# Optimization experiments

Hardware: AMD Instinct MI355X
Metric: run time of the kernel (lower is better)

## Reference

```python
import jax, jax.numpy as jnp
import numpy as np

H = 8          # query heads
HKV = 4        # kv heads
D = 256        # head dim
GROUPS = H // HKV
HIDDEN = 2304
WINDOW = 2048  # sliding window
SOFTCAP = 50.0
SCALE = (HIDDEN // H) ** -0.5  # query_pre_attn_scalar uses hidden//heads, not head_dim
NEG = -1e9
ROPE_BASE = 10000.0


def _rope_tables(L, offset=0, dtype=jnp.float32):
    inv_freq = 1.0 / (ROPE_BASE ** (jnp.arange(0, D, 2, dtype=jnp.float32) / D))
    t = jnp.arange(offset, offset + L, dtype=jnp.float32)
    freqs = jnp.outer(t, inv_freq)                    # [L, D/2]
    emb = jnp.concatenate([freqs, freqs], axis=-1)    # [L, D]
    return jnp.cos(emb).astype(dtype), jnp.sin(emb).astype(dtype)


def _rotate_half(x):
    x1, x2 = jnp.split(x, 2, axis=-1)
    return jnp.concatenate([-x2, x1], axis=-1)


def _apply_rope(x, cos, sin):
    # x: [B, h, L, D]; cos/sin: [L, D]
    return x * cos[None, None] + _rotate_half(x) * sin[None, None]


def setup_inputs() -> dict:
    key = jax.random.key(0)
    ks = jax.random.split(key, 5)
    B, L = 1, 4096
    x = jax.random.normal(ks[0], (B, L, HIDDEN), dtype=jnp.float32)
    wq = jax.random.normal(ks[1], (HIDDEN, H * D), dtype=jnp.float32) * 0.02
    wk = jax.random.normal(ks[2], (HIDDEN, HKV * D), dtype=jnp.float32) * 0.02
    wv = jax.random.normal(ks[3], (HIDDEN, HKV * D), dtype=jnp.float32) * 0.02
    wo = jax.random.normal(ks[4], (H * D, HIDDEN), dtype=jnp.float32) * 0.02
    # additive causal mask [1,1,L,L]
    causal = jnp.triu(jnp.full((L, L), NEG, dtype=jnp.float32), k=1)
    mask = causal[None, None]
    return {"x": x, "mask": mask, "wq": wq, "wk": wk, "wv": wv, "wo": wo}


def reference(x, mask, wq, wk, wv, wo):
    B, L, _ = x.shape
    q = (x @ wq).reshape(B, L, H, D).transpose(0, 2, 1, 3)     # [B,H,L,D]
    k = (x @ wk).reshape(B, L, HKV, D).transpose(0, 2, 1, 3)   # [B,HKV,L,D]
    v = (x @ wv).reshape(B, L, HKV, D).transpose(0, 2, 1, 3)

    cos, sin = _rope_tables(L, 0, q.dtype)
    q = _apply_rope(q, cos, sin)
    k = _apply_rope(k, cos, sin)

    # GQA: repeat_interleave kv heads
    k = jnp.repeat(k, GROUPS, axis=1)  # [B,H,L,D]
    v = jnp.repeat(v, GROUPS, axis=1)

    attn = jnp.einsum("bhqd,bhkd->bhqk", q, k) * SCALE
    attn = SOFTCAP * jnp.tanh(attn / SOFTCAP)
    attn = attn + mask

    kv_len = attn.shape[-1]
    if kv_len > WINDOW:  # sliding branch: keep only last WINDOW key columns
        col_keep = jnp.arange(kv_len) >= (kv_len - WINDOW)  # [kv_len]
        attn = jnp.where(col_keep[None, None, None, :], attn, NEG)

    attn = jax.nn.softmax(attn.astype(jnp.float32), axis=-1).astype(q.dtype)
    out = jnp.einsum("bhqk,bhkd->bhqd", attn, v)
    out = out.transpose(0, 2, 1, 3).reshape(B, L, H * D)
    return out @ wo
```

## Files before the change

kernel.cpp:

```cpp
#include <hip/hip_runtime.h>

typedef unsigned short u16;
typedef __bf16 bf16x8 __attribute__((ext_vector_type(8)));
typedef float floatx4 __attribute__((ext_vector_type(4)));
typedef unsigned short u16x4 __attribute__((ext_vector_type(4)));
typedef unsigned short u16x8 __attribute__((ext_vector_type(8)));

#define L_SEQ 4096
#define HID   2304
#define NH    8
#define NKV   4
#define HD    256
#define QDIM  2048
#define KVDIM 1024
#define SCALE_F 0.05892556509887896f

__device__ __forceinline__ u16 f2bf(float f) {
  unsigned u = __float_as_uint(f);
  u += 0x7FFFu + ((u >> 16) & 1u);
  return (u16)(u >> 16);
}
__device__ __forceinline__ float bf2f(u16 h) {
  return __uint_as_float(((unsigned)h) << 16);
}

__device__ __forceinline__ void async_load16(const u16* g, u16* lds_base) {
  __builtin_amdgcn_global_load_lds(
      (const __attribute__((address_space(1))) unsigned int*)g,
      (__attribute__((address_space(3))) unsigned int*)lds_base, 16, 0, 0);
}

__device__ __forceinline__ int swz(int m) { return (m + (m >> 2)) & 3; }

__global__ __launch_bounds__(256)
void cast_kernel(const float* __restrict__ in, u16* __restrict__ out, int n4) {
  int i = blockIdx.x * 256 + threadIdx.x;
  if (i < n4) {
    float4 v = *reinterpret_cast<const float4*>(&in[(size_t)i * 4]);
    u16x4 o;
    o[0] = f2bf(v.x); o[1] = f2bf(v.y); o[2] = f2bf(v.z); o[3] = f2bf(v.w);
    *reinterpret_cast<u16x4*>(&out[(size_t)i * 4]) = o;
  }
}

__global__ __launch_bounds__(256)
void transpose_kernel(const float* __restrict__ wq, const float* __restrict__ wk,
                      const float* __restrict__ wv, const float* __restrict__ wo,
                      u16* __restrict__ wqkvT, u16* __restrict__ woT) {
  const int z = blockIdx.z;
  const float* W; u16* WT; int K, N;
  if (z == 0)      { W = wq; WT = wqkvT;                            K = HID;  N = QDIM; }
  else if (z == 1) { W = wk; WT = wqkvT + (size_t)QDIM * HID;       K = HID;  N = KVDIM; }
  else if (z == 2) { W = wv; WT = wqkvT + (size_t)(QDIM + KVDIM) * HID; K = HID; N = KVDIM; }
  else             { W = wo; WT = woT;                              K = QDIM; N = HID; }
  const int n0 = blockIdx.x * 32, k0 = blockIdx.y * 32;
  if (n0 >= N || k0 >= K) return;
  __shared__ u16 t[32][33];
  const int c = threadIdx.x & 31, r4 = (threadIdx.x >> 5) * 4;
#pragma unroll
  for (int i = 0; i < 4; ++i)
    t[r4 + i][c] = f2bf(W[(size_t)(k0 + r4 + i) * N + n0 + c]);
  __syncthreads();
#pragma unroll
  for (int i = 0; i < 4; ++i)
    WT[(size_t)(n0 + r4 + i) * K + k0 + c] = t[c][r4 + i];
}

#define G256_NT 36

#define G256_BARRIER() __builtin_amdgcn_s_barrier()
#define G256_SCHEDB()  __builtin_amdgcn_sched_barrier(0)

#define G256_STAGE(bb, X, kh, tt)                                              \
  {                                                                            \
    const u16* g = (X) ? BT + (size_t)(n0 + w * 32 + srow) * HID               \
                       : A + (size_t)(m0 + w * 32 + srow) * HID;               \
    const int kc = (tt) * 64 + (kh) * 32 + schk;                               \
    async_load16(g + kc, &lds[bb][X][kh][(w * 32) * 32]);                      \
    async_load16(g + 16 * HID + kc, &lds[bb][X][kh][(w * 32 + 16) * 32]);      \
  }

#define G256_RD_B(dst, bb, kk)                                                 \
  {                                                                            \
    const u16* Bk = &lds[bb][1][kk][0];                                        \
    _Pragma("unroll") for (int nt = 0; nt < 4; ++nt)                           \
        dst[nt] = *reinterpret_cast<const bf16x8*>(                            \
            &Bk[(wn + nt * 16 + l16) * 32 + rsw]);                             \
  }

#define G256_RD_A(dst, bb, kk, ch)                                             \
  {                                                                            \
    const u16* Ak = &lds[bb][0][kk][0];                                        \
    _Pragma("unroll") for (int mt = 0; mt < 4; ++mt)                           \
        dst[mt] = *reinterpret_cast<const bf16x8*>(                            \
            &Ak[(wm + ((ch) * 4 + mt) * 16 + l16) * 32 + rsw]);                \
  }

#define G256_MFMA(ch, AA, BB)                                                  \
  {                                                                            \
    __builtin_amdgcn_s_setprio(1);                                             \
    _Pragma("unroll") for (int mt = 0; mt < 4; ++mt)                           \
        _Pragma("unroll") for (int nt = 0; nt < 4; ++nt)                       \
            acc[(ch) * 4 + mt][nt] = __builtin_amdgcn_mfma_f32_16x16x32_bf16(  \
                AA[mt], BB[nt], acc[(ch) * 4 + mt][nt], 0, 0, 0);              \
    __builtin_amdgcn_s_setprio(0);                                             \
  }

#define G256_VMCNT4() __asm__ volatile("s_waitcnt vmcnt(4)")
#define G256_VMCNT0() __asm__ volatile("s_waitcnt vmcnt(0)")

__global__ __launch_bounds__(512)
void gemm256_kernel(const u16* __restrict__ A, const u16* __restrict__ BT,
                    u16* __restrict__ C) {
  __shared__ __align__(16) u16 lds[2][2][2][256 * 32];

  const int tid  = threadIdx.x;
  const int lane = tid & 63;
  const int w    = tid >> 6;
  const int l16  = lane & 15;
  const int quad = lane >> 4;
  const int wm   = (w >> 2) * 128;
  const int wn   = (w & 3) * 64;

  const int srow = lane >> 2;
  const int schk = (((lane & 3) ^ ((lane >> 3) & 3))) * 8;
  const int rsw = ((quad ^ ((l16 >> 1) & 3))) * 8;

  const int bid = blockIdx.x;
  const int id  = (bid & 7) * 20 + (bid >> 3);

  int m0, n0, region;
  if (id < 64)      { region = 0; n0 = (id & 7) * 256;          m0 = 2048 + (id >> 3) * 256; }
  else if (id < 96) { region = 1; const int i = id - 64;
                      n0 = 2048 + (i & 3) * 256;                m0 = 2048 + (i >> 2) * 256; }
  else              { region = 2; const int i = id - 96;
                      n0 = 3072 + (i & 3) * 256;                m0 = (i >> 2) * 256; }

  floatx4 acc[8][4];
#pragma unroll
  for (int i = 0; i < 8; ++i)
#pragma unroll
    for (int j = 0; j < 4; ++j) acc[i][j] = (floatx4){0.f, 0.f, 0.f, 0.f};

  G256_STAGE(0, 0, 0, 0); G256_STAGE(0, 1, 0, 0);
  G256_STAGE(0, 0, 1, 0); G256_STAGE(0, 1, 1, 0);
  G256_STAGE(1, 0, 0, 1); G256_STAGE(1, 1, 0, 1);
  G256_VMCNT4();
  G256_BARRIER();

#pragma unroll 2
  for (int t = 0; t < G256_NT; ++t) {
    const int bb = t & 1;
    bf16x8 a_cur[4], b_cur[4], a_hi0[4], a_lo1[4], b1[4], a_hi1[4];

    G256_RD_A(a_cur, bb, 0, 0);
    G256_RD_B(b_cur, bb, 0);
    G256_RD_A(a_hi0, bb, 0, 1);
    if (t + 1 < G256_NT) { G256_STAGE(bb ^ 1, 0, 1, t + 1); }
    G256_SCHEDB();
    G256_MFMA(0, a_cur, b_cur);
    G256_BARRIER();

    G256_RD_A(a_lo1, bb, 1, 0);
    G256_RD_B(b1, bb, 1);
    if (t + 1 < G256_NT) { G256_STAGE(bb ^ 1, 1, 1, t + 1); }
    G256_SCHEDB();
    G256_MFMA(1, a_hi0, b_cur);
    G256_BARRIER();

    G256_RD_A(a_hi1, bb, 1, 1);
    if (t + 2 < G256_NT) { G256_STAGE(bb, 0, 0, t + 2); }
    G256_SCHEDB();
    G256_MFMA(0, a_lo1, b1);
    G256_BARRIER();

    if (t + 2 < G256_NT) { G256_STAGE(bb, 1, 0, t + 2); }
    G256_SCHEDB();
    G256_MFMA(1, a_hi1, b1);
    if (t < G256_NT - 2) { G256_VMCNT4(); }
    else                 { G256_VMCNT0(); }
    G256_BARRIER();
  }

#pragma unroll
  for (int mt = 0; mt < 8; ++mt)
#pragma unroll
    for (int nt = 0; nt < 4; ++nt) {
      const int mbase = m0 + wm + mt * 16 + quad * 4;
      const int n = n0 + wn + nt * 16 + l16;
      if (region == 0) {
        const size_t base = (size_t)(n >> 8) * L_SEQ * HD + (n & 255);
#pragma unroll
        for (int r = 0; r < 4; ++r)
          C[base + (size_t)(mbase + r) * HD] = f2bf(acc[mt][nt][r]);
      } else if (region == 1) {
        const int nk2 = n - QDIM;
        const size_t base = (size_t)NH * L_SEQ * HD +
                            (size_t)(nk2 >> 8) * L_SEQ * HD + (nk2 & 255);
#pragma unroll
        for (int r = 0; r < 4; ++r)
          C[base + (size_t)(mbase + r) * HD] = f2bf(acc[mt][nt][r]);
      } else {
        const int nv = n - QDIM - KVDIM;
        u16x4 o;
#pragma unroll
        for (int r = 0; r < 4; ++r) o[r] = f2bf(acc[mt][nt][r]);
        *reinterpret_cast<u16x4*>(
            &C[(size_t)(NH + NKV) * L_SEQ * HD +
               ((size_t)(nv >> 8) * HD + (nv & 255)) * L_SEQ + mbase]) = o;
      }
    }
}

template<int MODE>
__global__ __launch_bounds__(256)
void gemm_kernel(const u16* __restrict__ A, const u16* __restrict__ BT,
                 void* __restrict__ Cp, int N, int K) {
  __shared__ __align__(16) u16 Alds[128][32];
  __shared__ __align__(16) u16 Blds[128][32];

  const int tid  = threadIdx.x;
  const int lane = tid & 63;
  const int w    = tid >> 6;
  const int wm   = (w >> 1) * 64;
  const int wn   = (w & 1) * 64;
  const int l16  = lane & 15;
  const int quad = lane >> 4;

  int m0, n0;
  if (MODE == 0) {
    const int id = blockIdx.x;
    if (id < 256)      { n0 = (id & 15) * 128;                 m0 = 2048 + (id >> 4) * 128; }
    else if (id < 384) { const int i2 = id - 256;
                         n0 = 2048 + (i2 & 7) * 128;           m0 = 2048 + (i2 >> 3) * 128; }
    else               { const int i3 = id - 384;
                         n0 = 3072 + (i3 & 7) * 128;           m0 = (i3 >> 3) * 128; }
  } else {
    m0 = blockIdx.y * 128;
    n0 = blockIdx.x * 128;
  }

  const int srow_in = lane >> 2;
  const int schunk  = lane & 3;

  floatx4 acc[4][4];
#pragma unroll
  for (int i = 0; i < 4; ++i)
#pragma unroll
    for (int j = 0; j < 4; ++j) acc[i][j] = (floatx4){0.f, 0.f, 0.f, 0.f};

  const int nk = K >> 5;
  for (int kt = 0; kt < nk; ++kt) {
    __syncthreads();
#pragma unroll
    for (int p = 0; p < 2; ++p) {
      const int row = w * 32 + p * 16 + srow_in;
      const int ce  = schunk ^ swz(row);
      async_load16(&A[(size_t)(m0 + row) * K + kt * 32 + ce * 8], &Alds[w * 32 + p * 16][0]);
      async_load16(&BT[(size_t)(n0 + row) * K + kt * 32 + ce * 8], &Blds[w * 32 + p * 16][0]);
    }
    __syncthreads();

    bf16x8 a[4], b[4];
#pragma unroll
    for (int mt = 0; mt < 4; ++mt) {
      const int row = wm + mt * 16 + l16;
      a[mt] = *reinterpret_cast<const bf16x8*>(&Alds[row][(quad ^ swz(row)) * 8]);
    }
#pragma unroll
    for (int nt = 0; nt < 4; ++nt) {
      const int row = wn + nt * 16 + l16;
      b[nt] = *reinterpret_cast<const bf16x8*>(&Blds[row][(quad ^ swz(row)) * 8]);
    }
#pragma unroll
    for (int mt = 0; mt < 4; ++mt)
#pragma unroll
      for (int nt = 0; nt < 4; ++nt)
        acc[mt][nt] = __builtin_amdgcn_mfma_f32_16x16x32_bf16(a[mt], b[nt], acc[mt][nt], 0, 0, 0);
  }

#pragma unroll
  for (int mt = 0; mt < 4; ++mt)
#pragma unroll
    for (int nt = 0; nt < 4; ++nt) {
      const int mbase = m0 + wm + mt * 16 + quad * 4;
      const int n = n0 + wn + nt * 16 + l16;
      if (MODE == 0) {
        u16* C = (u16*)Cp;
        if (n < QDIM) {
          const size_t base = (size_t)(n >> 8) * L_SEQ * HD + (n & 255);
#pragma unroll
          for (int r = 0; r < 4; ++r)
            C[base + (size_t)(mbase + r) * HD] = f2bf(acc[mt][nt][r]);
        } else if (n < QDIM + KVDIM) {
          const int nk2 = n - QDIM;
          const size_t base = (size_t)NH * L_SEQ * HD +
                              (size_t)(nk2 >> 8) * L_SEQ * HD + (nk2 & 255);
#pragma unroll
          for (int r = 0; r < 4; ++r)
            C[base + (size_t)(mbase + r) * HD] = f2bf(acc[mt][nt][r]);
        } else {
          const int nv = n - QDIM - KVDIM;
          u16x4 o;
#pragma unroll
          for (int r = 0; r < 4; ++r) o[r] = f2bf(acc[mt][nt][r]);
          *reinterpret_cast<u16x4*>(
              &C[(size_t)(NH + NKV) * L_SEQ * HD +
                 ((size_t)(nv >> 8) * HD + (nv & 255)) * L_SEQ + mbase]) = o;
        }
      } else {
        float* C = (float*)Cp;
#pragma unroll
        for (int r = 0; r < 4; ++r)
          C[(size_t)(mbase + r) * N + n] = acc[mt][nt][r];
      }
    }
}

__global__ __launch_bounds__(128)
void rope_kernel(u16* __restrict__ qb, u16* __restrict__ kb) {
  const int l  = 2048 + blockIdx.x;
  const int hh = blockIdx.y;
  u16* base = (hh < NH) ? qb + ((size_t)hh * L_SEQ + l) * HD
                        : kb + ((size_t)(hh - NH) * L_SEQ + l) * HD;
  const int d = threadIdx.x;
  const float invf = exp2f((float)d * (-13.287712379549449f / 128.0f));
  const float ang = (float)l * invf;
  float s, c;
  sincosf(ang, &s, &c);
  const float x1 = bf2f(base[d]);
  const float x2 = bf2f(base[d + 128]);
  base[d]       = f2bf(x1 * c - x2 * s);
  base[d + 128] = f2bf(x2 * c + x1 * s);
}

__global__ __launch_bounds__(256)
void meanv_kernel(const u16* __restrict__ vt, float* __restrict__ mv) {
  const int row  = blockIdx.x * 4 + (threadIdx.x >> 6);
  const int lane = threadIdx.x & 63;
  const u16* p = vt + (size_t)row * L_SEQ;
  float s = 0.f;
#pragma unroll
  for (int c = 0; c < 8; ++c) {
    u16x8 v = *reinterpret_cast<const u16x8*>(&p[(c * 64 + lane) * 8]);
#pragma unroll
    for (int j = 0; j < 8; ++j) s += bf2f(v[j]);
  }
#pragma unroll
  for (int off = 32; off > 0; off >>= 1) s += __shfl_xor(s, off, 64);
  if (lane == 0) mv[row] = s * (1.0f / 4096.0f);
}

__global__ __launch_bounds__(256)
void rowvec_part_kernel(const float* __restrict__ mv, const float* __restrict__ wo,
                        float* __restrict__ rpart) {
  const int j = blockIdx.x * 256 + threadIdx.x;
  const int c0 = blockIdx.y * 128;
  float acc = 0.f;
#pragma unroll 4
  for (int cc = 0; cc < 128; ++cc) {
    const int c = c0 + cc;
    const float a = mv[((c >> 9) << 8) | (c & 255)];
    acc += a * wo[(size_t)c * HID + j];
  }
  rpart[blockIdx.y * HID + j] = acc;
}

__global__ __launch_bounds__(256)
void rowvec_reduce_kernel(const float* __restrict__ rpart, float* __restrict__ r) {
  const int j = blockIdx.x * 256 + threadIdx.x;
  float s = 0.f;
#pragma unroll
  for (int p = 0; p < 16; ++p) s += rpart[p * HID + j];
  r[j] = s;
}

__global__ __launch_bounds__(256)
void bcast_out_kernel(const float* __restrict__ r, float* __restrict__ out) {
  const int idx = blockIdx.x * 256 + threadIdx.x;
  const int col4 = idx % 576;
  *reinterpret_cast<float4*>(&out[(size_t)idx * 4]) =
      *reinterpret_cast<const float4*>(&r[col4 * 4]);
}

__global__ __launch_bounds__(256)
void attn_kernel(const u16* __restrict__ qb, const u16* __restrict__ kb,
                 const u16* __restrict__ vt, float* __restrict__ Opart,
                 float* __restrict__ lpart) {
  const int s = blockIdx.x;
  const int pr = blockIdx.y;
  const int h = blockIdx.z;
  const int kvh = h >> 1;
  const int tid = threadIdx.x;
  const int w = tid >> 6, lane = tid & 63;
  const int l16 = lane & 15, quad = lane >> 4;

  __shared__ __align__(16) u16 Klds[32 * 256];
  __shared__ __align__(16) u16 Vlds[256 * 32];
  __shared__ u16 Plds[4][16][40];

  const int n_a = 2 * pr + 2;
  const int lo = (66 * s) >> 2;
  const int hi = (66 * (s + 1)) >> 2;

  const int r_lo[2] = {lo, (lo > n_a) ? lo : n_a};
  const int r_hi[2] = {(hi < n_a) ? hi : n_a, hi};
  const int r_t[2]  = {32 + pr, 63 - pr};
  const int r_off[2] = {64, 64 - n_a};

  const u16* kg0 = kb + (size_t)kvh * L_SEQ * HD;
  const u16* vg0 = vt + (size_t)kvh * HD * L_SEQ;

  for (int run = 0; run < 2; ++run) {
    if (r_lo[run] >= r_hi[run]) continue;
    const int t  = r_t[run];
    const int q0 = t * 64 + w * 16;

    bf16x8 aq[8];
    {
      const u16* qr = qb + ((size_t)h * L_SEQ + q0 + l16) * HD + quad * 8;
#pragma unroll
      for (int f = 0; f < 8; ++f)
        aq[f] = *reinterpret_cast<const bf16x8*>(&qr[f * 32]);
    }

    floatx4 acc[16];
#pragma unroll
    for (int i = 0; i < 16; ++i) acc[i] = (floatx4){0.f, 0.f, 0.f, 0.f};
    float lsum[4] = {0.f, 0.f, 0.f, 0.f};

    for (int g = r_lo[run]; g < r_hi[run]; ++g) {
      const int kt = r_off[run] + g;
      __syncthreads();
      {
        const u16* kg = kg0 + (size_t)kt * 32 * HD;
#pragma unroll
        for (int p = 0; p < 4; ++p) {
          const int r   = w * 8 + p * 2 + (lane >> 5);
          const int pos = lane & 31;
          const int c   = (pos & 24) | ((pos ^ r) & 7);
          async_load16(&kg[(size_t)r * HD + c * 8], &Klds[(w * 8 + p * 2) * 256]);
        }
        const u16* vg = vg0 + kt * 32;
#pragma unroll
        for (int j = 0; j < 4; ++j) {
          const int m  = w * 32 + j * 8 + (lane >> 3);
          const int p  = lane & 7;
          const int c2 = p ^ (m & 7);
          const int r  = m * 2 + (c2 >> 2);
          async_load16(&vg[(size_t)r * L_SEQ + (c2 & 3) * 8], &Vlds[(w * 32 + j * 8) * 64]);
        }
      }
      __syncthreads();

      floatx4 sa[2] = {(floatx4){0.f, 0.f, 0.f, 0.f}, (floatx4){0.f, 0.f, 0.f, 0.f}};
#pragma unroll
      for (int nt = 0; nt < 2; ++nt) {
        const int row = nt * 16 + l16;
#pragma unroll
        for (int f = 0; f < 8; ++f) {
          const int c   = f * 4 + quad;
          const int pos = (c & 24) | ((c ^ row) & 7);
          bf16x8 bk = *reinterpret_cast<const bf16x8*>(&Klds[row * 256 + pos * 8]);
          sa[nt] = __builtin_amdgcn_mfma_f32_16x16x32_bf16(aq[f], bk, sa[nt], 0, 0, 0);
        }
      }
#pragma unroll
      for (int nt = 0; nt < 2; ++nt) {
        const int key = kt * 32 + nt * 16 + l16;
#pragma unroll
        for (int r = 0; r < 4; ++r) {
          const float x = sa[nt][r] * SCALE_F;
          const float capm50 = -100.0f / (__expf(x * 0.04f) + 1.0f);
          float p = __expf(capm50);
          const int qq = q0 + quad * 4 + r;
          p = (key <= qq) ? p : 0.0f;
          lsum[r] += p;
          Plds[w][quad * 4 + r][nt * 16 + l16] = f2bf(p);
        }
      }
      __asm__ volatile("s_waitcnt lgkmcnt(0)" ::: "memory");
      bf16x8 ap = *reinterpret_cast<const bf16x8*>(&Plds[w][l16][quad * 8]);
#pragma unroll
      for (int dt = 0; dt < 16; ++dt) {
        const int rV = dt * 16 + l16;
        const int m  = rV >> 1;
        const int p  = ((rV & 1) * 4 + quad) ^ (m & 7);
        bf16x8 bv = *reinterpret_cast<const bf16x8*>(&Vlds[m * 64 + p * 8]);
        acc[dt] = __builtin_amdgcn_mfma_f32_16x16x32_bf16(ap, bv, acc[dt], 0, 0, 0);
      }
    }

#pragma unroll
    for (int r = 0; r < 4; ++r) {
      float l = lsum[r];
      l += __shfl_xor(l, 1); l += __shfl_xor(l, 2);
      l += __shfl_xor(l, 4); l += __shfl_xor(l, 8);
      lsum[r] = l;
    }
    const int ql0 = q0 - 2048 + quad * 4;
#pragma unroll
    for (int r = 0; r < 4; ++r) {
      float* orow = Opart + (((size_t)s * NH + h) * 2048 + ql0 + r) * HD + l16;
#pragma unroll
      for (int dt = 0; dt < 16; ++dt) orow[dt * 16] = acc[dt][r];
      if (l16 == 0) lpart[((size_t)s * NH + h) * 2048 + ql0 + r] = lsum[r];
    }
  }
}

__global__ __launch_bounds__(256)
void combine_kernel(const float* __restrict__ Opart, const float* __restrict__ lpart,
                    u16* __restrict__ ab) {
  const int idx4 = blockIdx.x * 256 + threadIdx.x;
  const int d4 = (idx4 & 63) * 4;
  const int ql = (idx4 >> 6) & 2047;
  const int h  = idx4 >> 17;
  const int qtile = ql >> 6;
  const bool role_a = qtile < 16;
  const int pr = role_a ? qtile : 31 - qtile;
  const int lo_s[4] = {0, 16, 33, 49};
  const int hi_s[4] = {16, 33, 49, 66};

  float4 o = {0.f, 0.f, 0.f, 0.f};
  float l = 0.f;
#pragma unroll
  for (int s = 0; s < 4; ++s) {
    const bool valid = role_a ? (lo_s[s] < 2 * pr + 2) : (hi_s[s] > 2 * pr + 2);
    if (valid) {
      float4 v = *reinterpret_cast<const float4*>(
          &Opart[(((size_t)s * NH + h) * 2048 + ql) * HD + d4]);
      o.x += v.x; o.y += v.y; o.z += v.z; o.w += v.w;
      l += lpart[((size_t)s * NH + h) * 2048 + ql];
    }
  }
  const float inv = 1.0f / l;
  u16x4 ov;
  ov[0] = f2bf(o.x * inv); ov[1] = f2bf(o.y * inv);
  ov[2] = f2bf(o.z * inv); ov[3] = f2bf(o.w * inv);
  *reinterpret_cast<u16x4*>(&ab[(size_t)(2048 + ql) * QDIM + h * HD + d4]) = ov;
}

extern "C" void kernel_launch(void* const* d_in, const int* in_sizes, int n_in,
                              void* d_out, int out_size, void* d_ws, size_t ws_size,
                              hipStream_t stream) {
  const float* x  = (const float*)d_in[0];
  const float* wq = (const float*)d_in[2];
  const float* wk = (const float*)d_in[3];
  const float* wv = (const float*)d_in[4];
  const float* wo = (const float*)d_in[5];
  float* out = (float*)d_out;

  u16* qb  = (u16*)d_ws;
  u16* kb  = qb  + (size_t)NH  * L_SEQ * HD;
  u16* vtb = kb  + (size_t)NKV * L_SEQ * HD;
  u16* ab  = vtb + (size_t)NKV * L_SEQ * HD;
  u16* xb  = ab  + (size_t)L_SEQ * QDIM;
  u16* wqkvT = xb + (size_t)L_SEQ * HID;
  u16* woT = wqkvT + (size_t)(QDIM + 2 * KVDIM) * HID;
  float* Opart = (float*)(woT + (size_t)HID * QDIM);
  float* lpart = Opart + (size_t)4 * NH * 2048 * HD;
  float* mv    = lpart + (size_t)4 * NH * 2048;
  float* rpart = mv + 1024;
  float* rvec  = rpart + 16 * HID;

  cast_kernel<<<dim3(L_SEQ * HID / 4 / 256), 256, 0, stream>>>(x, xb, L_SEQ * HID / 4);
  transpose_kernel<<<dim3(72, 72, 4), 256, 0, stream>>>(wq, wk, wv, wo, wqkvT, woT);

  gemm256_kernel<<<dim3(160), 512, 0, stream>>>(xb, wqkvT, qb);
  rope_kernel<<<dim3(L_SEQ / 2, NH + NKV), 128, 0, stream>>>(qb, kb);
  meanv_kernel<<<dim3(256), 256, 0, stream>>>(vtb, mv);

  rowvec_part_kernel<<<dim3(9, 16), 256, 0, stream>>>(mv, wo, rpart);
  rowvec_reduce_kernel<<<dim3(9), 256, 0, stream>>>(rpart, rvec);
  bcast_out_kernel<<<dim3(2048 * 576 / 256), 256, 0, stream>>>(rvec, out);

  attn_kernel<<<dim3(4, 16, NH), 256, 0, stream>>>(qb, kb, vtb, Opart, lpart);
  combine_kernel<<<dim3(4096), 256, 0, stream>>>(Opart, lpart, ab);

  gemm_kernel<1><<<dim3(HID / 128, 2048 / 128), 256, 0, stream>>>(
      ab + (size_t)2048 * QDIM, woT, out + (size_t)2048 * HID, HID, QDIM);
}
```

Measured before the change: 368.2 us.

## Double-buffer K/V tiles in attention kernel with async prefetch two stages ahead

Splits the K and V shared-memory tiles into two buffers and issues the async global-to-LDS loads for tile g+2 while tile g is being computed. Synchronisation now uses explicit vmcnt waits plus raw barriers in place of two __syncthreads per iteration. The goal is to hide global-memory latency behind the MFMA work. In exchange it doubles LDS use, which can lower occupancy, and it relies on hand-counted vmcnt values that could race if the load count per stage changes. It also adds an empty asm constraint to pin the Q fragments in registers.

```diff
diff --git a/kernel.cpp b/kernel.cpp
--- a/kernel.cpp
+++ b/kernel.cpp
@@ -383,6 +383,28 @@
       *reinterpret_cast<const float4*>(&r[col4 * 4]);
 }
 
+#define ATT_STAGE(g_, buf_)                                                    \
+  {                                                                            \
+    const int kt_ = r_off[run] + (g_);                                         \
+    const u16* kg_ = kg0 + (size_t)kt_ * 32 * HD;                              \
+    _Pragma("unroll") for (int p_ = 0; p_ < 4; ++p_) {                         \
+      const int r_   = w * 8 + p_ * 2 + (lane >> 5);                           \
+      const int pos_ = lane & 31;                                              \
+      const int c_   = (pos_ & 24) | ((pos_ ^ r_) & 7);                        \
+      async_load16(&kg_[(size_t)r_ * HD + c_ * 8],                             \
+                   &Klds[buf_][(w * 8 + p_ * 2) * 256]);                       \
+    }                                                                          \
+    const u16* vg_ = vg0 + kt_ * 32;                                           \
+    _Pragma("unroll") for (int j_ = 0; j_ < 4; ++j_) {                         \
+      const int m_  = w * 32 + j_ * 8 + (lane >> 3);                           \
+      const int p2_ = lane & 7;                                                \
+      const int c2_ = p2_ ^ (m_ & 7);                                          \
+      const int r2_ = m_ * 2 + (c2_ >> 2);                                     \
+      async_load16(&vg_[(size_t)r2_ * L_SEQ + (c2_ & 3) * 8],                  \
+                   &Vlds[buf_][(w * 32 + j_ * 8) * 64]);                       \
+    }                                                                          \
+  }
+
 __global__ __launch_bounds__(256)
 void attn_kernel(const u16* __restrict__ qb, const u16* __restrict__ kb,
                  const u16* __restrict__ vt, float* __restrict__ Opart,
@@ -395,8 +417,8 @@
   const int w = tid >> 6, lane = tid & 63;
   const int l16 = lane & 15, quad = lane >> 4;
 
-  __shared__ __align__(16) u16 Klds[32 * 256];
-  __shared__ __align__(16) u16 Vlds[256 * 32];
+  __shared__ __align__(16) u16 Klds[2][32 * 256];
+  __shared__ __align__(16) u16 Vlds[2][256 * 32];
   __shared__ u16 Plds[4][16][40];
 
   const int n_a = 2 * pr + 2;
@@ -415,6 +437,7 @@
     if (r_lo[run] >= r_hi[run]) continue;
     const int t  = r_t[run];
     const int q0 = t * 64 + w * 16;
+    const int glo = r_lo[run], ghi = r_hi[run];
 
     bf16x8 aq[8];
     {
@@ -422,36 +445,30 @@
 #pragma unroll
       for (int f = 0; f < 8; ++f)
         aq[f] = *reinterpret_cast<const bf16x8*>(&qr[f * 32]);
-    }
+#pragma unroll
+      for (int f = 0; f < 8; ++f) {
+        floatx4& t4 = reinterpret_cast<floatx4&>(aq[f]);
+        __asm__ volatile("" : "+v"(t4));
+      }
+    }
+
+    ATT_STAGE(glo, 0);
+    if (glo + 1 < ghi) ATT_STAGE(glo + 1, 1);
 
     floatx4 acc[16];
 #pragma unroll
     for (int i = 0; i < 16; ++i) acc[i] = (floatx4){0.f, 0.f, 0.f, 0.f};
     float lsum[4] = {0.f, 0.f, 0.f, 0.f};
 
-    for (int g = r_lo[run]; g < r_hi[run]; ++g) {
+    for (int g = glo; g < ghi; ++g) {
+      const int cur = (g - glo) & 1;
       const int kt = r_off[run] + g;
-      __syncthreads();
-      {
-        const u16* kg = kg0 + (size_t)kt * 32 * HD;
-#pragma unroll
-        for (int p = 0; p < 4; ++p) {
-          const int r   = w * 8 + p * 2 + (lane >> 5);
-          const int pos = lane & 31;
-          const int c   = (pos & 24) | ((pos ^ r) & 7);
-          async_load16(&kg[(size_t)r * HD + c * 8], &Klds[(w * 8 + p * 2) * 256]);
-        }
-        const u16* vg = vg0 + kt * 32;
-#pragma unroll
-        for (int j = 0; j < 4; ++j) {
-          const int m  = w * 32 + j * 8 + (lane >> 3);
-          const int p  = lane & 7;
-          const int c2 = p ^ (m & 7);
-          const int r  = m * 2 + (c2 >> 2);
-          async_load16(&vg[(size_t)r * L_SEQ + (c2 & 3) * 8], &Vlds[(w * 32 + j * 8) * 64]);
-        }
-      }
-      __syncthreads();
+      if (g + 1 < ghi) { __asm__ volatile("s_waitcnt vmcnt(8)"); }
+      else             { __asm__ volatile("s_waitcnt vmcnt(0)"); }
+      __builtin_amdgcn_s_barrier();
+
+      const u16* Kb = &Klds[cur][0];
+      const u16* Vb = &Vlds[cur][0];
 
       floatx4 sa[2] = {(floatx4){0.f, 0.f, 0.f, 0.f}, (floatx4){0.f, 0.f, 0.f, 0.f}};
 #pragma unroll
@@ -461,7 +478,7 @@
         for (int f = 0; f < 8; ++f) {
           const int c   = f * 4 + quad;
           const int pos = (c & 24) | ((c ^ row) & 7);
-          bf16x8 bk = *reinterpret_cast<const bf16x8*>(&Klds[row * 256 + pos * 8]);
+          bf16x8 bk = *reinterpret_cast<const bf16x8*>(&Kb[row * 256 + pos * 8]);
           sa[nt] = __builtin_amdgcn_mfma_f32_16x16x32_bf16(aq[f], bk, sa[nt], 0, 0, 0);
         }
       }
@@ -486,9 +503,12 @@
         const int rV = dt * 16 + l16;
         const int m  = rV >> 1;
         const int p  = ((rV & 1) * 4 + quad) ^ (m & 7);
-        bf16x8 bv = *reinterpret_cast<const bf16x8*>(&Vlds[m * 64 + p * 8]);
+        bf16x8 bv = *reinterpret_cast<const bf16x8*>(&Vb[m * 64 + p * 8]);
         acc[dt] = __builtin_amdgcn_mfma_f32_16x16x32_bf16(ap, bv, acc[dt], 0, 0, 0);
       }
+
+      __builtin_amdgcn_s_barrier();
+      if (g + 2 < ghi) ATT_STAGE(g + 2, cur);
     }
 
 #pragma unroll
```

Measured after the change: 362.3 us. No clear change (-1.6%).
